# Kernel optimization log

Hardware: AMD Instinct MI355X
Metric: run time of the kernel (lower is better)

The kernel has to match this reference:

```python
import jax, jax.numpy as jnp
import numpy as np

DIM = 384
WIN = 64
HEADS = 12
B_ = 4096


def setup_inputs() -> dict:
    key = jax.random.key(0)
    k1, k2, k3, k4, k5 = jax.random.split(key, 5)
    x = jax.random.normal(k1, (B_, WIN, DIM), dtype=jnp.float32)
    # torch Linear weights: qkv.weight [3*dim, dim], proj.weight [dim, dim], proj.bias [dim]
    qkv_w = jax.random.normal(k2, (3 * DIM, DIM), dtype=jnp.float32) * (DIM ** -0.5)
    proj_w = jax.random.normal(k3, (DIM, DIM), dtype=jnp.float32) * (DIM ** -0.5)
    proj_b = jax.random.normal(k4, (DIM,), dtype=jnp.float32) * 0.02
    bias_table = jax.random.normal(k5, (2 * WIN - 1, HEADS), dtype=jnp.float32) * 0.02
    return {"x": x, "qkv_w": qkv_w, "proj_w": proj_w, "proj_b": proj_b,
            "bias_table": bias_table}


def reference(x, qkv_w, proj_w, proj_b, bias_table):
    B, N, C = x.shape
    H = HEADS
    hd = C // H
    scale = hd ** -0.5
    # qkv projection (torch: x @ W.T), split into q,k,v [B,H,N,hd]
    qkv = jnp.einsum('bnc,dc->bnd', x, qkv_w)
    qkv = qkv.reshape(B, N, 3, H, hd).transpose(2, 0, 3, 1, 4)
    q, k, v = qkv[0] * scale, qkv[1], qkv[2]
    attn = jnp.einsum('bhnd,bhmd->bhnm', q, k)  # [B,H,N,N]
    # relative position bias: index [N,N] into table [2W-1,H]
    coords = jnp.arange(N)
    rel_idx = coords[:, None] - coords[None, :] + (N - 1)  # [N,N]
    bias = bias_table[rel_idx]  # [N,N,H]
    attn = attn + bias.transpose(2, 0, 1)[None]
    attn = jax.nn.softmax(attn, axis=-1)
    out = jnp.einsum('bhnm,bhmd->bhnd', attn, v)
    out = out.transpose(0, 2, 1, 3).reshape(B, N, C)
    out = jnp.einsum('bnc,dc->bnd', out, proj_w) + proj_b
    return out
```

## Files before the change

kernel.cpp:

```cpp
#include <hip/hip_runtime.h>
#include <stdint.h>

#define DIM 384
#define WIN 64
#define HEADS 12
#define HD 32
#define NWIN 4096

typedef _Float16 f16;
typedef unsigned int u32;
typedef _Float16 half8 __attribute__((ext_vector_type(8)));
typedef _Float16 half4 __attribute__((ext_vector_type(4)));
typedef float floatx4 __attribute__((ext_vector_type(4)));

#define AS1 __attribute__((address_space(1)))
#define AS3 __attribute__((address_space(3)))

__device__ __forceinline__ void gl_lds16(const void* g, void* l) {
    __builtin_amdgcn_global_load_lds((const AS1 u32*)g, (AS3 u32*)l, 16, 0, 0);
}

__global__ void cvt_kernel(const float* __restrict__ in, f16* __restrict__ out, long n4) {
    long i = (long)blockIdx.x * blockDim.x + threadIdx.x;
    const long stride = (long)gridDim.x * blockDim.x;
    for (; i < n4; i += stride) {
        float4 v = ((const float4*)in)[i];
        half4 h;
        h[0] = (f16)v.x; h[1] = (f16)v.y; h[2] = (f16)v.z; h[3] = (f16)v.w;
        ((half4*)out)[i] = h;
    }
}

__global__ void pack_w_kernel(const float* __restrict__ w, f16* __restrict__ Bp) {
    const int t = blockIdx.x * 256 + threadIdx.x;
    const int colb = t / 9216;
    const int r1 = t % 9216;
    const int s = r1 / 768;
    const int r2 = r1 % 768;
    const int kc = r2 / 192, u = r2 % 192;
    const float* sp = w + (size_t)(colb * 192 + u) * DIM + s * 32 + kc * 8;
    float4 a = *(const float4*)sp;
    float4 b = *(const float4*)(sp + 4);
    half8 o;
    o[0] = (f16)a.x; o[1] = (f16)a.y; o[2] = (f16)a.z; o[3] = (f16)a.w;
    o[4] = (f16)b.x; o[5] = (f16)b.y; o[6] = (f16)b.z; o[7] = (f16)b.w;
    *(half8*)(Bp + (size_t)t * 8) = o;
}

__global__ void __launch_bounds__(512, 2)
qkv_kernel(const float* __restrict__ X32, const f16* __restrict__ Bp,
           f16* __restrict__ q_arr, f16* __restrict__ k_arr,
           f16* __restrict__ v_int, int nwg)
{
    __shared__ __align__(16) f16 xa[2][2][256][32];
    __shared__ __align__(16) f16 ldsB[3][12288];

    int lin = blockIdx.x;
    int nlin = lin;
    if ((nwg & 7) == 0) nlin = (lin & 7) * (nwg >> 3) + (lin >> 3);
    const int colb = nlin % 6, rowb = nlin / 6;
    const int row0 = rowb * 256;

    const int tid = threadIdx.x;
    const int wave = tid >> 6, lane = tid & 63;
    const int g = lane >> 4, c = lane & 15;
    const int wm = wave >> 1, wn = wave & 1;

    floatx4 acc[4][6] = {};
    float4 rA[8];

    auto loadA = [&](int t) {
#pragma unroll
        for (int r = 0; r < 8; ++r) {
            const int i = r * 512 + tid;
            const int row = i >> 4, kq = i & 15;
            rA[r] = *(const float4*)(X32 + (size_t)(row0 + row) * DIM + t * 64 + kq * 4);
        }
    };
    auto writeA = [&](int t) {
#pragma unroll
        for (int r = 0; r < 8; ++r) {
            const int i = r * 512 + tid;
            const int row = i >> 4, kq = i & 15;
            const int ks = kq >> 3, kq2 = kq & 7;
            const int sl = (kq2 >> 1) ^ ((row >> 1) & 3);
            half4 h;
            h[0] = (f16)rA[r].x; h[1] = (f16)rA[r].y;
            h[2] = (f16)rA[r].z; h[3] = (f16)rA[r].w;
            *(half4*)&xa[t & 1][ks][row][sl * 8 + (kq2 & 1) * 4] = h;
        }
    };
    auto stageB = [&](int t) {
        f16* db = &ldsB[t % 3][0];
#pragma unroll
        for (int r = 0; r < 3; ++r) {
            const int ch = r * 512 + tid;
            const int ss = ch / 768, rem = ch % 768;
            const f16* src = Bp + ((size_t)colb * 12 + (2 * t + ss)) * 6144 + (size_t)rem * 8;
            gl_lds16(src, db + ch * 8);
        }
    };

    loadA(0); stageB(0); stageB(1);
    writeA(0);
    loadA(1);

#pragma unroll
    for (int t = 0; t < 6; ++t) {
        asm volatile("s_waitcnt vmcnt(11)" ::: "memory");
        asm volatile("s_waitcnt lgkmcnt(0)" ::: "memory");
        __builtin_amdgcn_sched_barrier(0);
        __builtin_amdgcn_s_barrier();
        __builtin_amdgcn_sched_barrier(0);
        if (t < 4) stageB(t + 2);

        const f16* bb = &ldsB[t % 3][0];
#pragma unroll
        for (int ks = 0; ks < 2; ++ks) {
            half8 af[4], bf[6];
#pragma unroll
            for (int mi = 0; mi < 4; ++mi) {
                const int row = wm * 64 + mi * 16 + c;
                const int sl = g ^ ((row >> 1) & 3);
                af[mi] = *(const half8*)&xa[t & 1][ks][row][sl * 8];
            }
#pragma unroll
            for (int ni = 0; ni < 6; ++ni) {
                const int u = wn * 96 + ni * 16 + c;
                bf[ni] = *(const half8*)(bb + ks * 6144 + g * 1536 + u * 8);
            }
#pragma unroll
            for (int mi = 0; mi < 4; ++mi)
#pragma unroll
                for (int ni = 0; ni < 6; ++ni)
                    acc[mi][ni] = __builtin_amdgcn_mfma_f32_16x16x32_f16(
                        af[mi], bf[ni], acc[mi][ni], 0, 0, 0);
        }
        if (t < 5) writeA(t + 1);
        if (t < 4) loadA(t + 2);
    }

    const int which = colb >> 1;
    const int dbase = (colb & 1) * 192;
    const int b0 = rowb * 4 + wm;
    if (which < 2) {
        f16* dst = which ? k_arr : q_arr;
        const float sc = which ? 1.0f : 0.17677669529663687f;
#pragma unroll
        for (int ni = 0; ni < 6; ++ni) {
            const int d = dbase + wn * 96 + ni * 16 + c;
            const int h = d >> 5, e = d & 31;
            f16* base = dst + (size_t)(b0 * HEADS + h) * (WIN * HD) + e;
#pragma unroll
            for (int mi = 0; mi < 4; ++mi)
#pragma unroll
                for (int j = 0; j < 4; ++j) {
                    const int n = mi * 16 + g * 4 + j;
                    base[(size_t)n * HD] = (f16)(acc[mi][ni][j] * sc);
                }
        }
    } else {
#pragma unroll
        for (int ni = 0; ni < 6; ++ni) {
            const int d = dbase + wn * 96 + ni * 16 + c;
            const int h = d >> 5, e = d & 31;
            f16* vb = v_int + (size_t)(b0 * HEADS + h) * (WIN * HD);
#pragma unroll
            for (int mi = 0; mi < 4; ++mi) {
                const int n0 = mi * 16 + g * 4;
                half4 pk;
#pragma unroll
                for (int j = 0; j < 4; ++j) pk[j] = (f16)acc[mi][ni][j];
                *(half4*)(vb + (n0 >> 3) * 256 + e * 8 + (n0 & 7)) = pk;
            }
        }
    }
}

__global__ void proj_kernel(const f16* __restrict__ A, const f16* __restrict__ Bw,
                            float* __restrict__ outp, const float* __restrict__ proj_b,
                            int nwg)
{
    __shared__ __align__(16) f16 lds[3][2][4][128][8];

    int lin = blockIdx.x;
    int nlin = lin;
    if ((nwg & 7) == 0) nlin = (lin & 7) * (nwg >> 3) + (lin >> 3);
    const int colb = nlin % 3, rowb = nlin / 3;
    const int col0 = colb * 128, row0 = rowb * 128;

    const int tid = threadIdx.x;
    const int wave = tid >> 6, lane = tid & 63;
    const int g = lane >> 4, c = lane & 15;
    const int wm = wave >> 1, wn = wave & 1;

    floatx4 acc[4][4] = {};

    auto stage = [&](int t) {
        const int k0 = t * 32;
#pragma unroll
        for (int r = 0; r < 4; ++r) {
            const int u = wave + r * 4;
            const int isB = u >> 3;
            const int uu = u & 7;
            const int kc = uu >> 1, m0 = (uu & 1) * 64;
            const f16* src = (isB ? Bw + (size_t)(col0 + m0 + lane) * DIM
                                  : A  + (size_t)(row0 + m0 + lane) * DIM)
                             + k0 + kc * 8;
            gl_lds16(src, &lds[t % 3][isB][kc][m0][0]);
        }
    };

    stage(0); stage(1);

#pragma unroll
    for (int s = 0; s < 12; ++s) {
        if (s < 11) asm volatile("s_waitcnt vmcnt(4)" ::: "memory");
        else        asm volatile("s_waitcnt vmcnt(0)" ::: "memory");
        asm volatile("s_waitcnt lgkmcnt(0)" ::: "memory");
        __builtin_amdgcn_sched_barrier(0);
        __builtin_amdgcn_s_barrier();
        __builtin_amdgcn_sched_barrier(0);
        if (s < 10) stage(s + 2);

        half8 af[4], bf[4];
#pragma unroll
        for (int i = 0; i < 4; ++i) {
            af[i] = *(const half8*)&lds[s % 3][0][g][wm * 64 + i * 16 + c][0];
            bf[i] = *(const half8*)&lds[s % 3][1][g][wn * 64 + i * 16 + c][0];
        }
#pragma unroll
        for (int mi = 0; mi < 4; ++mi)
#pragma unroll
            for (int ni = 0; ni < 4; ++ni)
                acc[mi][ni] = __builtin_amdgcn_mfma_f32_16x16x32_f16(
                    af[mi], bf[ni], acc[mi][ni], 0, 0, 0);
    }

#pragma unroll
    for (int ni = 0; ni < 4; ++ni) {
        const int d = col0 + wn * 64 + ni * 16 + c;
        const float pb = proj_b[d];
#pragma unroll
        for (int mi = 0; mi < 4; ++mi)
#pragma unroll
            for (int j = 0; j < 4; ++j) {
                const size_t trow = (size_t)row0 + wm * 64 + mi * 16 + g * 4 + j;
                outp[trow * DIM + d] = acc[mi][ni][j] + pb;
            }
    }
}

__global__ void attn_kernel(const f16* __restrict__ q_arr, const f16* __restrict__ k_arr,
                            const f16* __restrict__ v_int,
                            const float* __restrict__ bias_table,
                            f16* __restrict__ attn_out)
{
    const int bid = blockIdx.x;
    const int bw = bid / HEADS, h = bid % HEADS;
    const f16* q = q_arr + (size_t)bid * (WIN * HD);
    const f16* k = k_arr + (size_t)bid * (WIN * HD);
    const f16* v = v_int + (size_t)bid * (WIN * HD);

    const int tid = threadIdx.x;
    const int w = tid >> 6, lane = tid & 63;
    const int g = lane >> 4, c = lane & 15;

    __shared__ float bias_lds[2 * WIN - 1];
    __shared__ __align__(16) f16 p_lds[8][64][8];

    for (int i = tid; i < 2 * WIN - 1; i += 256)
        bias_lds[i] = bias_table[(size_t)i * HEADS + h];
    __syncthreads();

    half8 qa = *(const half8*)(q + (16 * w + c) * HD + g * 8);
    floatx4 s[4];
#pragma unroll
    for (int t = 0; t < 4; ++t) {
        half8 kb = *(const half8*)(k + (16 * t + c) * HD + g * 8);
        floatx4 z = {};
        s[t] = __builtin_amdgcn_mfma_f32_16x16x32_f16(qa, kb, z, 0, 0, 0);
    }

    float pr[4][4];
#pragma unroll
    for (int j = 0; j < 4; ++j) {
        const int n = 16 * w + g * 4 + j;
        float mx = -1e30f;
#pragma unroll
        for (int t = 0; t < 4; ++t) {
            const int m = 16 * t + c;
            pr[j][t] = s[t][j] + bias_lds[n - m + 63];
            mx = fmaxf(mx, pr[j][t]);
        }
        mx = fmaxf(mx, __shfl_xor(mx, 1));
        mx = fmaxf(mx, __shfl_xor(mx, 2));
        mx = fmaxf(mx, __shfl_xor(mx, 4));
        mx = fmaxf(mx, __shfl_xor(mx, 8));
        float sum = 0.f;
#pragma unroll
        for (int t = 0; t < 4; ++t) { pr[j][t] = __expf(pr[j][t] - mx); sum += pr[j][t]; }
        sum += __shfl_xor(sum, 1);
        sum += __shfl_xor(sum, 2);
        sum += __shfl_xor(sum, 4);
        sum += __shfl_xor(sum, 8);
        const float r = 1.0f / sum;
#pragma unroll
        for (int t = 0; t < 4; ++t) {
            const int m = 16 * t + c;
            p_lds[m >> 3][n][m & 7] = (f16)(pr[j][t] * r);
        }
    }
    __syncthreads();

    half8 pa0 = *(const half8*)&p_lds[g][16 * w + c][0];
    half8 pa1 = *(const half8*)&p_lds[4 + g][16 * w + c][0];
    floatx4 o[2];
#pragma unroll
    for (int t = 0; t < 2; ++t) {
        half8 vb0 = *(const half8*)(v + g * 256 + (16 * t + c) * 8);
        half8 vb1 = *(const half8*)(v + (4 + g) * 256 + (16 * t + c) * 8);
        floatx4 z = {};
        o[t] = __builtin_amdgcn_mfma_f32_16x16x32_f16(pa0, vb0, z, 0, 0, 0);
        o[t] = __builtin_amdgcn_mfma_f32_16x16x32_f16(pa1, vb1, o[t], 0, 0, 0);
    }
#pragma unroll
    for (int t = 0; t < 2; ++t)
#pragma unroll
        for (int j = 0; j < 4; ++j) {
            const int n = 16 * w + g * 4 + j;
            attn_out[((size_t)bw * WIN + n) * DIM + h * HD + 16 * t + c] = (f16)o[t][j];
        }
}

extern "C" void kernel_launch(void* const* d_in, const int* in_sizes, int n_in,
                              void* d_out, int out_size, void* d_ws, size_t ws_size,
                              hipStream_t stream) {
    const float* x          = (const float*)d_in[0];
    const float* qkv_w      = (const float*)d_in[1];
    const float* proj_w     = (const float*)d_in[2];
    const float* proj_b     = (const float*)d_in[3];
    const float* bias_table = (const float*)d_in[4];
    float* out = (float*)d_out;
    (void)in_sizes; (void)n_in; (void)out_size;

    uintptr_t p = (uintptr_t)d_ws;
    auto carve = [&](size_t bytes) -> void* {
        uintptr_t q = p; p += (bytes + 255) & ~(size_t)255; return (void*)q;
    };
    f16* w16_proj = (f16*)carve((size_t)DIM * DIM * 2);
    f16* Bp       = (f16*)carve((size_t)6 * 12 * 768 * 8 * 2);
    const size_t fixed = p - (uintptr_t)d_ws;

    int CB = NWIN;
    while (CB > 16 && fixed + (size_t)CB * 196608 + 4096 > ws_size) CB >>= 1;

    f16* qa = (f16*)carve((size_t)CB * HEADS * WIN * HD * 2);
    f16* ka = (f16*)carve((size_t)CB * HEADS * WIN * HD * 2);
    f16* vi = (f16*)carve((size_t)CB * HEADS * WIN * HD * 2);
    f16* ao = (f16*)carve((size_t)CB * WIN * DIM * 2);

    cvt_kernel<<<dim3(64), dim3(256), 0, stream>>>(proj_w, w16_proj, (long)(DIM * DIM / 4));
    pack_w_kernel<<<dim3(216), dim3(256), 0, stream>>>(qkv_w, Bp);

    for (int c0 = 0; c0 < NWIN; c0 += CB) {
        const float* xc = x + (size_t)c0 * WIN * DIM;

        const int nwg1 = (CB * WIN / 256) * 6;
        qkv_kernel<<<dim3(nwg1), dim3(512), 0, stream>>>(xc, Bp, qa, ka, vi, nwg1);

        attn_kernel<<<dim3(CB * HEADS), dim3(256), 0, stream>>>(qa, ka, vi, bias_table, ao);

        const int nwg2 = (CB * WIN / 128) * 3;
        proj_kernel<<<dim3(nwg2), dim3(256), 0, stream>>>(ao, w16_proj,
                                                          out + (size_t)c0 * WIN * DIM, proj_b, nwg2);
    }
}
```

Before: 852.9 us.

## Fuse window attention and output projection into one kernel per window

Replaces the separate attention kernel (one block per window-head) and tiled projection GEMM with a single kernel per window. Each of 4 waves runs attention for 3 heads, writes the per-window attention output into LDS, then the block multiplies it by the projection weight, streamed in 32-wide K slices, and adds the bias. This removes the global round trip of the attention output and one launch. In exchange each block re-reads the full projection weight, LDS use per block is large (about 80 KB), and the softmax probabilities go through a global scratch buffer instead of LDS.

```diff
diff --git a/kernel.cpp b/kernel.cpp
--- a/kernel.cpp
+++ b/kernel.cpp
@@ -177,160 +177,181 @@
     }
 }
 
-__global__ void proj_kernel(const f16* __restrict__ A, const f16* __restrict__ Bw,
-                            float* __restrict__ outp, const float* __restrict__ proj_b,
-                            int nwg)
+__global__ void __launch_bounds__(256, 2)
+attnproj_kernel(const f16* __restrict__ q_arr, const f16* __restrict__ k_arr,
+                const f16* __restrict__ v_int, const float* __restrict__ bias_table,
+                const f16* __restrict__ Wp, const float* __restrict__ proj_b,
+                f16* __restrict__ pbuf, float* __restrict__ outp)
 {
-    __shared__ __align__(16) f16 lds[3][2][4][128][8];
-
-    int lin = blockIdx.x;
-    int nlin = lin;
-    if ((nwg & 7) == 0) nlin = (lin & 7) * (nwg >> 3) + (lin >> 3);
-    const int colb = nlin % 3, rowb = nlin / 3;
-    const int col0 = colb * 128, row0 = rowb * 128;
-
+    __shared__ __align__(16) f16 ao[64][392];
+    __shared__ __align__(16) f16 Wst[12288];
+    __shared__ float bl[12 * 128];
+
+    const int lw = blockIdx.x;
     const int tid = threadIdx.x;
-    const int wave = tid >> 6, lane = tid & 63;
+    const int wv = tid >> 6, lane = tid & 63;
     const int g = lane >> 4, c = lane & 15;
-    const int wm = wave >> 1, wn = wave & 1;
-
-    floatx4 acc[4][4] = {};
-
-    auto stage = [&](int t) {
-        const int k0 = t * 32;
-#pragma unroll
-        for (int r = 0; r < 4; ++r) {
-            const int u = wave + r * 4;
-            const int isB = u >> 3;
-            const int uu = u & 7;
-            const int kc = uu >> 1, m0 = (uu & 1) * 64;
-            const f16* src = (isB ? Bw + (size_t)(col0 + m0 + lane) * DIM
-                                  : A  + (size_t)(row0 + m0 + lane) * DIM)
-                             + k0 + kc * 8;
-            gl_lds16(src, &lds[t % 3][isB][kc][m0][0]);
-        }
-    };
-
-    stage(0); stage(1);
-
-#pragma unroll
-    for (int s = 0; s < 12; ++s) {
-        if (s < 11) asm volatile("s_waitcnt vmcnt(4)" ::: "memory");
-        else        asm volatile("s_waitcnt vmcnt(0)" ::: "memory");
-        asm volatile("s_waitcnt lgkmcnt(0)" ::: "memory");
+
+    for (int i = tid; i < 127 * HEADS; i += 256) {
+        const int pos = i / 12, h = i % 12;
+        bl[h * 128 + pos] = bias_table[i];
+    }
+
+    auto stageW = [&](int t) {
+#pragma unroll
+        for (int r = 0; r < 6; ++r) {
+            const int ch = r * 256 + tid;
+            const int u = ch >> 2, kc = ch & 3;
+            gl_lds16(Wp + (size_t)u * DIM + t * 32 + kc * 8, &Wst[ch * 8]);
+        }
+    };
+    stageW(0);
+    __syncthreads();
+
+    char* pbc = (char*)pbuf + ((size_t)lw * 4 + wv) * 8192;
+#pragma unroll 1
+    for (int hh = 0; hh < 3; ++hh) {
+        const int h = wv * 3 + hh;
+        const int dh = h * HD;
+        const f16* qh = q_arr + ((size_t)lw * HEADS + h) * 2048;
+        const f16* kh = k_arr + ((size_t)lw * HEADS + h) * 2048;
+        const f16* vh = v_int + ((size_t)lw * HEADS + h) * 2048;
+
+        half8 qaf[4], kbf[4];
+#pragma unroll
+        for (int t = 0; t < 4; ++t) {
+            qaf[t] = *(const half8*)(qh + (16 * t + c) * HD + g * 8);
+            kbf[t] = *(const half8*)(kh + (16 * t + c) * HD + g * 8);
+        }
+        floatx4 S[4][4];
+#pragma unroll
+        for (int nt = 0; nt < 4; ++nt)
+#pragma unroll
+            for (int mt = 0; mt < 4; ++mt) {
+                floatx4 z = {0.f, 0.f, 0.f, 0.f};
+                S[nt][mt] = __builtin_amdgcn_mfma_f32_16x16x32_f16(qaf[nt], kbf[mt], z, 0, 0, 0);
+            }
+
+        const float* bh = bl + h * 128 + 63;
+#pragma unroll
+        for (int nt = 0; nt < 4; ++nt)
+#pragma unroll
+            for (int j = 0; j < 4; ++j) {
+                const int n = 16 * nt + 4 * g + j;
+                float mx = -1e30f;
+#pragma unroll
+                for (int mt = 0; mt < 4; ++mt) {
+                    const int m = 16 * mt + c;
+                    S[nt][mt][j] += bh[n - m];
+                    mx = fmaxf(mx, S[nt][mt][j]);
+                }
+                mx = fmaxf(mx, __shfl_xor(mx, 1));
+                mx = fmaxf(mx, __shfl_xor(mx, 2));
+                mx = fmaxf(mx, __shfl_xor(mx, 4));
+                mx = fmaxf(mx, __shfl_xor(mx, 8));
+                float sum = 0.f;
+#pragma unroll
+                for (int mt = 0; mt < 4; ++mt) {
+                    S[nt][mt][j] = __expf(S[nt][mt][j] - mx);
+                    sum += S[nt][mt][j];
+                }
+                sum += __shfl_xor(sum, 1);
+                sum += __shfl_xor(sum, 2);
+                sum += __shfl_xor(sum, 4);
+                sum += __shfl_xor(sum, 8);
+                const float ri = 1.0f / sum;
+#pragma unroll
+                for (int mt = 0; mt < 4; ++mt) {
+                    const int m = 16 * mt + c;
+                    *(f16*)(pbc + n * 128 + m * 2) = (f16)(S[nt][mt][j] * ri);
+                }
+            }
+
+        asm volatile("s_waitcnt vmcnt(0)" ::: "memory");
+        __builtin_amdgcn_sched_barrier(0);
+
+        half8 pa[4][2], vb[2][2];
+#pragma unroll
+        for (int mi = 0; mi < 4; ++mi)
+#pragma unroll
+            for (int ks = 0; ks < 2; ++ks)
+                pa[mi][ks] = *(const half8*)(pbc + (16 * mi + c) * 128 + (ks * 32 + 8 * g) * 2);
+#pragma unroll
+        for (int t2 = 0; t2 < 2; ++t2)
+#pragma unroll
+            for (int ks = 0; ks < 2; ++ks)
+                vb[t2][ks] = *(const half8*)(vh + (ks * 4 + g) * 256 + (16 * t2 + c) * 8);
+        floatx4 O[4][2];
+#pragma unroll
+        for (int mi = 0; mi < 4; ++mi)
+#pragma unroll
+            for (int t2 = 0; t2 < 2; ++t2) O[mi][t2] = floatx4{0.f, 0.f, 0.f, 0.f};
+#pragma unroll
+        for (int ks = 0; ks < 2; ++ks)
+#pragma unroll
+            for (int mi = 0; mi < 4; ++mi)
+#pragma unroll
+                for (int t2 = 0; t2 < 2; ++t2)
+                    O[mi][t2] = __builtin_amdgcn_mfma_f32_16x16x32_f16(
+                        pa[mi][ks], vb[t2][ks], O[mi][t2], 0, 0, 0);
+#pragma unroll
+        for (int mi = 0; mi < 4; ++mi)
+#pragma unroll
+            for (int t2 = 0; t2 < 2; ++t2)
+#pragma unroll
+                for (int j = 0; j < 4; ++j) {
+                    const int n = 16 * mi + 4 * g + j;
+                    ao[n][dh + 16 * t2 + c] = (f16)O[mi][t2][j];
+                }
+    }
+    __syncthreads();
+
+    floatx4 acc[4][6];
+#pragma unroll
+    for (int mi = 0; mi < 4; ++mi)
+#pragma unroll
+        for (int ni = 0; ni < 6; ++ni) acc[mi][ni] = floatx4{0.f, 0.f, 0.f, 0.f};
+
+#pragma unroll 1
+    for (int t = 0; t < 12; ++t) {
+        asm volatile("s_waitcnt vmcnt(0)" ::: "memory");
         __builtin_amdgcn_sched_barrier(0);
         __builtin_amdgcn_s_barrier();
         __builtin_amdgcn_sched_barrier(0);
-        if (s < 10) stage(s + 2);
-
-        half8 af[4], bf[4];
-#pragma unroll
-        for (int i = 0; i < 4; ++i) {
-            af[i] = *(const half8*)&lds[s % 3][0][g][wm * 64 + i * 16 + c][0];
-            bf[i] = *(const half8*)&lds[s % 3][1][g][wn * 64 + i * 16 + c][0];
-        }
-#pragma unroll
-        for (int mi = 0; mi < 4; ++mi)
-#pragma unroll
-            for (int ni = 0; ni < 4; ++ni)
+
+        half8 af[4], bf[6];
+#pragma unroll
+        for (int mi = 0; mi < 4; ++mi)
+            af[mi] = *(const half8*)&ao[16 * mi + c][t * 32 + g * 8];
+#pragma unroll
+        for (int ni = 0; ni < 6; ++ni) {
+            const int u = wv * 96 + ni * 16 + c;
+            bf[ni] = *(const half8*)&Wst[u * 32 + g * 8];
+        }
+#pragma unroll
+        for (int mi = 0; mi < 4; ++mi)
+#pragma unroll
+            for (int ni = 0; ni < 6; ++ni)
                 acc[mi][ni] = __builtin_amdgcn_mfma_f32_16x16x32_f16(
                     af[mi], bf[ni], acc[mi][ni], 0, 0, 0);
-    }
-
-#pragma unroll
-    for (int ni = 0; ni < 4; ++ni) {
-        const int d = col0 + wn * 64 + ni * 16 + c;
+
+        __builtin_amdgcn_s_barrier();
+        __builtin_amdgcn_sched_barrier(0);
+        if (t < 11) stageW(t + 1);
+    }
+
+#pragma unroll
+    for (int ni = 0; ni < 6; ++ni) {
+        const int d = wv * 96 + ni * 16 + c;
         const float pb = proj_b[d];
 #pragma unroll
         for (int mi = 0; mi < 4; ++mi)
 #pragma unroll
             for (int j = 0; j < 4; ++j) {
-                const size_t trow = (size_t)row0 + wm * 64 + mi * 16 + g * 4 + j;
-                outp[trow * DIM + d] = acc[mi][ni][j] + pb;
-            }
-    }
-}
-
-__global__ void attn_kernel(const f16* __restrict__ q_arr, const f16* __restrict__ k_arr,
-                            const f16* __restrict__ v_int,
-                            const float* __restrict__ bias_table,
-                            f16* __restrict__ attn_out)
-{
-    const int bid = blockIdx.x;
-    const int bw = bid / HEADS, h = bid % HEADS;
-    const f16* q = q_arr + (size_t)bid * (WIN * HD);
-    const f16* k = k_arr + (size_t)bid * (WIN * HD);
-    const f16* v = v_int + (size_t)bid * (WIN * HD);
-
-    const int tid = threadIdx.x;
-    const int w = tid >> 6, lane = tid & 63;
-    const int g = lane >> 4, c = lane & 15;
-
-    __shared__ float bias_lds[2 * WIN - 1];
-    __shared__ __align__(16) f16 p_lds[8][64][8];
-
-    for (int i = tid; i < 2 * WIN - 1; i += 256)
-        bias_lds[i] = bias_table[(size_t)i * HEADS + h];
-    __syncthreads();
-
-    half8 qa = *(const half8*)(q + (16 * w + c) * HD + g * 8);
-    floatx4 s[4];
-#pragma unroll
-    for (int t = 0; t < 4; ++t) {
-        half8 kb = *(const half8*)(k + (16 * t + c) * HD + g * 8);
-        floatx4 z = {};
-        s[t] = __builtin_amdgcn_mfma_f32_16x16x32_f16(qa, kb, z, 0, 0, 0);
-    }
-
-    float pr[4][4];
-#pragma unroll
-    for (int j = 0; j < 4; ++j) {
-        const int n = 16 * w + g * 4 + j;
-        float mx = -1e30f;
-#pragma unroll
-        for (int t = 0; t < 4; ++t) {
-            const int m = 16 * t + c;
-            pr[j][t] = s[t][j] + bias_lds[n - m + 63];
-            mx = fmaxf(mx, pr[j][t]);
-        }
-        mx = fmaxf(mx, __shfl_xor(mx, 1));
-        mx = fmaxf(mx, __shfl_xor(mx, 2));
-        mx = fmaxf(mx, __shfl_xor(mx, 4));
-        mx = fmaxf(mx, __shfl_xor(mx, 8));
-        float sum = 0.f;
-#pragma unroll
-        for (int t = 0; t < 4; ++t) { pr[j][t] = __expf(pr[j][t] - mx); sum += pr[j][t]; }
-        sum += __shfl_xor(sum, 1);
-        sum += __shfl_xor(sum, 2);
-        sum += __shfl_xor(sum, 4);
-        sum += __shfl_xor(sum, 8);
-        const float r = 1.0f / sum;
-#pragma unroll
-        for (int t = 0; t < 4; ++t) {
-            const int m = 16 * t + c;
-            p_lds[m >> 3][n][m & 7] = (f16)(pr[j][t] * r);
-        }
-    }
-    __syncthreads();
-
-    half8 pa0 = *(const half8*)&p_lds[g][16 * w + c][0];
-    half8 pa1 = *(const half8*)&p_lds[4 + g][16 * w + c][0];
-    floatx4 o[2];
-#pragma unroll
-    for (int t = 0; t < 2; ++t) {
-        half8 vb0 = *(const half8*)(v + g * 256 + (16 * t + c) * 8);
-        half8 vb1 = *(const half8*)(v + (4 + g) * 256 + (16 * t + c) * 8);
-        floatx4 z = {};
-        o[t] = __builtin_amdgcn_mfma_f32_16x16x32_f16(pa0, vb0, z, 0, 0, 0);
-        o[t] = __builtin_amdgcn_mfma_f32_16x16x32_f16(pa1, vb1, o[t], 0, 0, 0);
-    }
-#pragma unroll
-    for (int t = 0; t < 2; ++t)
-#pragma unroll
-        for (int j = 0; j < 4; ++j) {
-            const int n = 16 * w + g * 4 + j;
-            attn_out[((size_t)bw * WIN + n) * DIM + h * HD + 16 * t + c] = (f16)o[t][j];
-        }
+                const int n = 16 * mi + 4 * g + j;
+                outp[((size_t)lw * WIN + n) * DIM + d] = acc[mi][ni][j] + pb;
+            }
+    }
 }
 
 extern "C" void kernel_launch(void* const* d_in, const int* in_sizes, int n_in,
@@ -353,12 +374,12 @@
     const size_t fixed = p - (uintptr_t)d_ws;
 
     int CB = NWIN;
-    while (CB > 16 && fixed + (size_t)CB * 196608 + 4096 > ws_size) CB >>= 1;
-
-    f16* qa = (f16*)carve((size_t)CB * HEADS * WIN * HD * 2);
-    f16* ka = (f16*)carve((size_t)CB * HEADS * WIN * HD * 2);
-    f16* vi = (f16*)carve((size_t)CB * HEADS * WIN * HD * 2);
-    f16* ao = (f16*)carve((size_t)CB * WIN * DIM * 2);
+    while (CB > 16 && fixed + (size_t)CB * 180224 + 4096 > ws_size) CB >>= 1;
+
+    f16* qa   = (f16*)carve((size_t)CB * HEADS * WIN * HD * 2);
+    f16* ka   = (f16*)carve((size_t)CB * HEADS * WIN * HD * 2);
+    f16* vi   = (f16*)carve((size_t)CB * HEADS * WIN * HD * 2);
+    f16* pbuf = (f16*)carve((size_t)CB * 4 * 8192);
 
     cvt_kernel<<<dim3(64), dim3(256), 0, stream>>>(proj_w, w16_proj, (long)(DIM * DIM / 4));
     pack_w_kernel<<<dim3(216), dim3(256), 0, stream>>>(qkv_w, Bp);
@@ -369,10 +390,8 @@
         const int nwg1 = (CB * WIN / 256) * 6;
         qkv_kernel<<<dim3(nwg1), dim3(512), 0, stream>>>(xc, Bp, qa, ka, vi, nwg1);
 
-        attn_kernel<<<dim3(CB * HEADS), dim3(256), 0, stream>>>(qa, ka, vi, bias_table, ao);
-
-        const int nwg2 = (CB * WIN / 128) * 3;
-        proj_kernel<<<dim3(nwg2), dim3(256), 0, stream>>>(ao, w16_proj,
-                                                          out + (size_t)c0 * WIN * DIM, proj_b, nwg2);
-    }
-}
+        attnproj_kernel<<<dim3(CB), dim3(256), 0, stream>>>(qa, ka, vi, bias_table,
+                                                            w16_proj, proj_b, pbuf,
+                                                            out + (size_t)c0 * WIN * DIM);
+    }
+}
```

Result: no change. 861.5 us (+1.0%).
